# Kernel tuning notes

Measured on AMD Instinct MI355X. Metric: run time of the kernel, lower is better.

Reference implementation:

```python
import jax, jax.numpy as jnp
import numpy as np

EMBED_DIM = 512
NUM_HEADS = 8
HEAD_DIM = EMBED_DIM // NUM_HEADS  # 64


def setup_inputs() -> dict:
    key = jax.random.key(0)
    ks = jax.random.split(key, 9)
    B, N, E, H, D = 4, 1024, EMBED_DIM, NUM_HEADS, HEAD_DIM
    s = 1.0 / np.sqrt(E)  # ~ nn.Linear init scale
    x = jax.random.normal(ks[0], (B, N, E), dtype=jnp.float32)
    # weights stored as (in, out): y = x @ W + b (same math as torch x @ W.T)
    Wq = jax.random.uniform(ks[1], (E, E), jnp.float32, -s, s)
    bq = jax.random.uniform(ks[2], (E,), jnp.float32, -s, s)
    Wk = jax.random.uniform(ks[3], (E, E), jnp.float32, -s, s)
    bk = jax.random.uniform(ks[4], (E,), jnp.float32, -s, s)
    Wv = jax.random.uniform(ks[5], (E, E), jnp.float32, -s, s)
    bv = jax.random.uniform(ks[6], (E,), jnp.float32, -s, s)
    Wg = jax.random.uniform(ks[7], (E, H * D * D), jnp.float32, -s, s)
    bg = jax.random.uniform(ks[8], (H * D * D,), jnp.float32, -s, s)
    return {"x": x, "Wq": Wq, "bq": bq, "Wk": Wk, "bk": bk,
            "Wv": Wv, "bv": bv, "Wg": Wg, "bg": bg}


def reference(x, Wq, bq, Wk, bk, Wv, bv, Wg, bg):
    B, N, E = x.shape
    H, D = NUM_HEADS, HEAD_DIM
    # per-token generated transform g: [B, N, H, D, D] (act = exact GELU)
    g = jax.nn.gelu(x @ Wg + bg, approximate=False).reshape(B, N, H, D, D)
    q = (x @ Wq + bq).reshape(B, N, H, D)
    k = (x @ Wk + bk).reshape(B, N, H, D)
    v = (x @ Wv + bv).reshape(B, N, H, D)
    # q' = q @ g  (per-token, per-head 1xD @ DxD)
    qg = jnp.einsum("bnhd,bnhde->bnhe", q, g)
    # attention scores (note: no 1/sqrt(d) scaling in the original)
    att = jnp.einsum("bnhe,bmhe->bhnm", qg, k)
    att = jax.nn.softmax(att, axis=-1)
    out = jnp.einsum("bhnm,bmhd->bnhd", att, v)
    return out.reshape(B, N, E)
```

## Files before the change

### kernel.cpp

```cpp
#include <hip/hip_runtime.h>
#include <math.h>

#define TOK   4096
#define EDIM  512
#define HEADS 8
#define DHEAD 64
#define GCOLS 32768

typedef unsigned short u16;
typedef _Float16 f16;
typedef __attribute__((ext_vector_type(8))) f16 f16x8;
typedef __attribute__((ext_vector_type(4))) f16 f16x4;
typedef __attribute__((ext_vector_type(4))) float f32x4;
typedef __attribute__((ext_vector_type(4))) unsigned short u16x4;

typedef const __attribute__((address_space(1))) void* gas_ptr;
typedef __attribute__((address_space(3))) void* las_ptr;

__device__ __forceinline__ void gll16(const void* g, void* lds) {
  __builtin_amdgcn_global_load_lds((gas_ptr)g, (las_ptr)lds, 16, 0, 0);
}

#define WAITV(N) asm volatile("s_waitcnt vmcnt(" #N ")" ::: "memory")
__device__ __forceinline__ void barrier_raw() { asm volatile("s_barrier" ::: "memory"); }

__device__ __forceinline__ u16 f2h_bits(float f) {
  union { f16 h; u16 u; } v; v.h = (f16)f;
  return v.u;
}

__device__ __forceinline__ float fast_gelu(float x) {
  float s = x * 0.7071067811865475f;
  float ax = fabsf(s);
  float t = __builtin_amdgcn_rcpf(1.0f + 0.3275911f * ax);
  float poly = t * (0.254829592f + t * (-0.284496736f + t * (1.421413741f +
               t * (-1.453152027f + t * 1.061405429f))));
  float e = __expf(-ax * ax);
  float r = 1.0f - poly * e;
  float erfv = copysignf(r, s);
  return 0.5f * x * (1.0f + erfv);
}

__global__ void cast_f16_k(const float* __restrict__ in, u16* __restrict__ out, int n) {
  int i = (blockIdx.x * blockDim.x + threadIdx.x) * 4;
  if (i + 3 < n) {
    float4 f = *(const float4*)(in + i);
    u16x4 h;
    h.x = f2h_bits(f.x); h.y = f2h_bits(f.y);
    h.z = f2h_bits(f.z); h.w = f2h_bits(f.w);
    *(u16x4*)(out + i) = h;
  }
}

__global__ void transpose_f16_k(const float* __restrict__ in, u16* __restrict__ out,
                                int K, int N) {
  __shared__ float tile[32][33];
  int n0 = blockIdx.x * 32, k0 = blockIdx.y * 32;
  int tx = threadIdx.x, ty = threadIdx.y;
  #pragma unroll
  for (int i = 0; i < 4; i++)
    tile[ty + i * 8][tx] = in[(size_t)(k0 + ty + i * 8) * N + n0 + tx];
  __syncthreads();
  #pragma unroll
  for (int i = 0; i < 4; i++)
    out[(size_t)(n0 + ty + i * 8) * K + k0 + tx] = f2h_bits(tile[tx][ty + i * 8]);
}

__global__ __launch_bounds__(256, 2) void qkv_gemm_k(
    const u16* __restrict__ xf, const u16* __restrict__ Wqt,
    const u16* __restrict__ Wkt, const u16* __restrict__ Wvt,
    const float* __restrict__ bq, const float* __restrict__ bk, const float* __restrict__ bv,
    u16* __restrict__ qho, u16* __restrict__ ko, u16* __restrict__ vTo) {
  __shared__ __align__(16) u16 As[2][16 * 512];
  __shared__ __align__(16) u16 Bs[2][16 * 512];
  const int which = blockIdx.z;
  const u16* Wt = which == 0 ? Wqt : (which == 1 ? Wkt : Wvt);
  const float* bias = which == 0 ? bq : (which == 1 ? bk : bv);
  const int m0 = blockIdx.x * 128;
  const int n0 = blockIdx.y * 128;
  const int tid = threadIdx.x;
  const int w = tid >> 6, lane = tid & 63, l15 = lane & 15, quad = lane >> 4;
  const int mhalf = w >> 1, nhalf = w & 1;

  f32x4 acc[4][4];
  #pragma unroll
  for (int i = 0; i < 4; i++)
    #pragma unroll
    for (int j = 0; j < 4; j++) acc[i][j] = f32x4{0.f, 0.f, 0.f, 0.f};

  auto stage = [&](int d, int kk) {
    #pragma unroll
    for (int i = 0; i < 8; i++) {
      int cb = w * 8 + i;
      if (cb < 16) {
        int ks = cb >> 3, mt = cb & 7;
        gll16(xf + (size_t)(m0 + mt * 16 + l15) * 512 + kk + ks * 32 + quad * 8,
              As[d] + cb * 512);
      } else {
        int bi = cb - 16, ks = bi >> 3, nt = bi & 7;
        gll16(Wt + (size_t)(n0 + nt * 16 + l15) * 512 + kk + ks * 32 + quad * 8,
              Bs[d] + bi * 512);
      }
    }
  };

  stage(0, 0);
  int cur = 0;
  for (int kt = 0; kt < 8; kt++) {
    if (kt < 7) { stage(cur ^ 1, (kt + 1) * 64); WAITV(8); }
    else        { WAITV(0); }
    barrier_raw();
    const u16* Asb = As[cur];
    const u16* Bsb = Bs[cur];
    #pragma unroll
    for (int ks = 0; ks < 2; ks++) {
      f16x8 a[4], b[4];
      #pragma unroll
      for (int mt = 0; mt < 4; mt++)
        a[mt] = *(const f16x8*)(Asb + (ks * 8 + mhalf * 4 + mt) * 512 + lane * 8);
      #pragma unroll
      for (int nt = 0; nt < 4; nt++)
        b[nt] = *(const f16x8*)(Bsb + (ks * 8 + nhalf * 4 + nt) * 512 + lane * 8);
      #pragma unroll
      for (int mt = 0; mt < 4; mt++)
        #pragma unroll
        for (int nt = 0; nt < 4; nt++)
          acc[mt][nt] = __builtin_amdgcn_mfma_f32_16x16x32_f16(a[mt], b[nt], acc[mt][nt], 0, 0, 0);
    }
    barrier_raw();
    cur ^= 1;
  }
  #pragma unroll
  for (int nt = 0; nt < 4; nt++) {
    int col = n0 + (nhalf * 4 + nt) * 16 + l15;
    float bia = bias[col];
    int h = col >> 6, d = col & 63;
    #pragma unroll
    for (int mt = 0; mt < 4; mt++) {
      #pragma unroll
      for (int r = 0; r < 4; r++) {
        int t = m0 + (mhalf * 4 + mt) * 16 + quad * 4 + r;
        int b_ = t >> 10, n = t & 1023;
        float val = acc[mt][nt][r] + bia;
        size_t idx = (((size_t)(b_ * 8 + h) * 1024) + n) * 64 + d;
        if (which == 0)      qho[idx] = f2h_bits(val);
        else if (which == 1) ko[idx] = f2h_bits(val);
        else                 vTo[(((size_t)(b_ * 8 + h) * 64) + d) * 1024 + n] = f2h_bits(val);
      }
    }
  }
}

__global__ __launch_bounds__(512, 2) void qg_fused_k(
    const u16* __restrict__ xf, const u16* __restrict__ Wgt,
    const float* __restrict__ bg, const u16* __restrict__ qh,
    u16* __restrict__ qg16) {
  __shared__ __align__(16) u16 As[2][16 * 512];
  __shared__ __align__(16) u16 Bs[2][32 * 512];
  __shared__ __align__(16) u16 Qs[128 * 64];
  __shared__ __align__(16) float bgs[4096];
  const int head = blockIdx.x & 7;
  const int t0 = (blockIdx.x >> 3) * 128;
  const int tid = threadIdx.x;
  const int w = tid >> 6, lane = tid & 63, l15 = lane & 15, quad = lane >> 4;
  const int mhalf = w >> 2;
  const int ntA = w & 3;
  const int b_ = t0 >> 10, nseq0 = t0 & 1023;
  const u16* qbase = qh + (((size_t)(b_ * 8 + head) * 1024) + nseq0) * 64;
  const float* bgbase = bg + head * 4096;

  #pragma unroll
  for (int i = 0; i < 2; i++) {
    int cb = w * 2 + i;
    gll16(qbase + (size_t)cb * 512 + (size_t)lane * 8, Qs + (size_t)cb * 512);
    gll16(bgbase + (size_t)cb * 256 + (size_t)lane * 4, bgs + (size_t)cb * 256);
  }

  auto stage = [&](int d, int s) {
    int jp = s >> 3, kk = (s & 7) << 6;
    int c0 = head * 4096 + jp * 256;
    #pragma unroll
    for (int i = 0; i < 6; i++) {
      int cb = w * 6 + i;
      if (cb < 16) {
        int ks = cb >> 3, mt = cb & 7;
        gll16(xf + (size_t)(t0 + mt * 16 + l15) * 512 + kk + ks * 32 + quad * 8,
              As[d] + cb * 512);
      } else {
        int bi = cb - 16, ks = bi >> 4, nt = bi & 15;
        gll16(Wgt + (size_t)(c0 + nt * 16 + l15) * 512 + kk + ks * 32 + quad * 8,
              Bs[d] + bi * 512);
      }
    }
  };

  f32x4 qg[4];
  #pragma unroll
  for (int i = 0; i < 4; i++) qg[i] = f32x4{0.f, 0.f, 0.f, 0.f};
  f32x4 zacc[4][4];
  #pragma unroll
  for (int i = 0; i < 4; i++)
    #pragma unroll
    for (int z = 0; z < 4; z++) zacc[i][z] = f32x4{0.f, 0.f, 0.f, 0.f};

  stage(0, 0);
  int cur = 0;
  for (int s = 0; s < 128; s++) {
    if (s < 127) { stage(cur ^ 1, s + 1); WAITV(6); }
    else         { WAITV(0); }
    barrier_raw();
    const u16* Asb = As[cur];
    const u16* Bsb = Bs[cur];
    #pragma unroll
    for (int ks = 0; ks < 2; ks++) {
      f16x8 a[4];
      #pragma unroll
      for (int mt = 0; mt < 4; mt++)
        a[mt] = *(const f16x8*)(Asb + (ks * 8 + mhalf * 4 + mt) * 512 + lane * 8);
      #pragma unroll
      for (int z = 0; z < 4; z++) {
        int nt = (z >> 1) * 8 + (z & 1) * 4 + ntA;
        f16x8 b = *(const f16x8*)(Bsb + (ks * 16 + nt) * 512 + lane * 8);
        #pragma unroll
        for (int mt = 0; mt < 4; mt++)
          zacc[mt][z] = __builtin_amdgcn_mfma_f32_16x16x32_f16(a[mt], b, zacc[mt][z], 0, 0, 0);
      }
    }
    if ((s & 7) == 7) {
      int jp = s >> 3;
      float bgv[4];
      #pragma unroll
      for (int z = 0; z < 4; z++) {
        int nt = (z >> 1) * 8 + (z & 1) * 4 + ntA;
        bgv[z] = bgs[jp * 256 + nt * 16 + l15];
      }
      const int d0 = 4 * jp;
      #pragma unroll
      for (int mt = 0; mt < 4; mt++) {
        #pragma unroll
        for (int r = 0; r < 4; r++) {
          int row = mhalf * 64 + mt * 16 + quad * 4 + r;
          f16x4 qp = *(const f16x4*)(Qs + row * 64 + d0);
          float g0 = fast_gelu(zacc[mt][0][r] + bgv[0]);
          float g1 = fast_gelu(zacc[mt][1][r] + bgv[1]);
          float g2 = fast_gelu(zacc[mt][2][r] + bgv[2]);
          float g3 = fast_gelu(zacc[mt][3][r] + bgv[3]);
          qg[mt][r] += (float)qp.x * g0 + (float)qp.y * g1 +
                       (float)qp.z * g2 + (float)qp.w * g3;
        }
      }
      #pragma unroll
      for (int i = 0; i < 4; i++)
        #pragma unroll
        for (int z = 0; z < 4; z++) zacc[i][z] = f32x4{0.f, 0.f, 0.f, 0.f};
    }
    barrier_raw();
    cur ^= 1;
  }
  const int eb = ntA * 16;
  #pragma unroll
  for (int mt = 0; mt < 4; mt++) {
    #pragma unroll
    for (int r = 0; r < 4; r++) {
      int t = t0 + mhalf * 64 + mt * 16 + quad * 4 + r;
      int bb = t >> 10, n = t & 1023;
      qg16[(((size_t)(bb * 8 + head) * 1024) + n) * 64 + eb + l15] = f2h_bits(qg[mt][r]);
    }
  }
}

__global__ __launch_bounds__(256, 2) void attn_k(
    const u16* __restrict__ qg16, const u16* __restrict__ kb,
    const u16* __restrict__ vTb, float* __restrict__ out) {
  __shared__ __align__(16) u16 Ks[2][8 * 512];
  __shared__ __align__(16) u16 Vs[2][8 * 512];
  __shared__ __align__(16) f16 Ps[4][16 * 72];
  const int idx = blockIdx.x;
  const int bh = idx & 31;
  const int qt = idx >> 5;
  const int b_ = bh >> 3, h = bh & 7;
  const int tid = threadIdx.x;
  const int w = tid >> 6, lane = tid & 63, l15 = lane & 15, quad = lane >> 4;

  const u16* qgB = qg16 + (size_t)bh * 1024 * 64;
  const u16* kB  = kb  + (size_t)bh * 1024 * 64;
  const u16* vB  = vTb + (size_t)bh * 64 * 1024;

  f16x8 aq[2];
  #pragma unroll
  for (int ks = 0; ks < 2; ks++)
    aq[ks] = *(const f16x8*)(qgB + (size_t)(qt * 64 + w * 16 + l15) * 64 + ks * 32 + quad * 8);

  f32x4 o[4];
  #pragma unroll
  for (int i = 0; i < 4; i++) o[i] = f32x4{0.f, 0.f, 0.f, 0.f};
  float m_old[4], l_old[4];
  #pragma unroll
  for (int r = 0; r < 4; r++) { m_old[r] = -1e30f; l_old[r] = 0.f; }

  auto stageKV = [&](int d, int kt) {
    #pragma unroll
    for (int i = 0; i < 2; i++) {
      int cb = w * 2 + i;
      int ks = cb >> 2, nt = cb & 3;
      gll16(kB + (size_t)(kt * 64 + nt * 16 + l15) * 64 + ks * 32 + quad * 8, Ks[d] + cb * 512);
      gll16(vB + (size_t)(nt * 16 + l15) * 1024 + kt * 64 + ks * 32 + quad * 8, Vs[d] + cb * 512);
    }
  };

  stageKV(0, 0);
  int cur = 0;
  for (int kt = 0; kt < 16; kt++) {
    if (kt < 15) { stageKV(cur ^ 1, kt + 1); WAITV(4); }
    else         { WAITV(0); }
    barrier_raw();
    f32x4 s[4];
    #pragma unroll
    for (int nt = 0; nt < 4; nt++) s[nt] = f32x4{0.f, 0.f, 0.f, 0.f};
    #pragma unroll
    for (int ks = 0; ks < 2; ks++)
      #pragma unroll
      for (int nt = 0; nt < 4; nt++) {
        f16x8 kf = *(const f16x8*)(Ks[cur] + (ks * 4 + nt) * 512 + lane * 8);
        s[nt] = __builtin_amdgcn_mfma_f32_16x16x32_f16(aq[ks], kf, s[nt], 0, 0, 0);
      }
    float rmax[4];
    #pragma unroll
    for (int r = 0; r < 4; r++)
      rmax[r] = fmaxf(fmaxf(s[0][r], s[1][r]), fmaxf(s[2][r], s[3][r]));
    #pragma unroll
    for (int off = 1; off < 16; off <<= 1)
      #pragma unroll
      for (int r = 0; r < 4; r++)
        rmax[r] = fmaxf(rmax[r], __shfl_xor(rmax[r], off));
    float alpha[4], rsum[4];
    #pragma unroll
    for (int r = 0; r < 4; r++) {
      float mn = fmaxf(m_old[r], rmax[r]);
      alpha[r] = __expf(m_old[r] - mn);
      m_old[r] = mn;
      rsum[r] = 0.f;
    }
    #pragma unroll
    for (int nt = 0; nt < 4; nt++)
      #pragma unroll
      for (int r = 0; r < 4; r++) {
        float p = __expf(s[nt][r] - m_old[r]);
        rsum[r] += p;
        Ps[w][(quad * 4 + r) * 72 + nt * 16 + l15] = (f16)p;
      }
    #pragma unroll
    for (int off = 1; off < 16; off <<= 1)
      #pragma unroll
      for (int r = 0; r < 4; r++)
        rsum[r] += __shfl_xor(rsum[r], off);
    #pragma unroll
    for (int r = 0; r < 4; r++) l_old[r] = l_old[r] * alpha[r] + rsum[r];
    #pragma unroll
    for (int nt = 0; nt < 4; nt++)
      #pragma unroll
      for (int r = 0; r < 4; r++) o[nt][r] *= alpha[r];
    #pragma unroll
    for (int ks = 0; ks < 2; ks++) {
      f16x8 pa = *(const f16x8*)(&Ps[w][l15 * 72 + ks * 32 + quad * 8]);
      #pragma unroll
      for (int nt = 0; nt < 4; nt++) {
        f16x8 vf = *(const f16x8*)(Vs[cur] + (ks * 4 + nt) * 512 + lane * 8);
        o[nt] = __builtin_amdgcn_mfma_f32_16x16x32_f16(pa, vf, o[nt], 0, 0, 0);
      }
    }
    barrier_raw();
    cur ^= 1;
  }
  #pragma unroll
  for (int r = 0; r < 4; r++) {
    float inv = 1.f / l_old[r];
    int n = qt * 64 + w * 16 + quad * 4 + r;
    #pragma unroll
    for (int nt = 0; nt < 4; nt++)
      out[((size_t)(b_ * 1024 + n)) * 512 + h * 64 + nt * 16 + l15] = o[nt][r] * inv;
  }
}

extern "C" void kernel_launch(void* const* d_in, const int* in_sizes, int n_in,
                              void* d_out, int out_size, void* d_ws, size_t ws_size,
                              hipStream_t stream) {
  const float* x  = (const float*)d_in[0];
  const float* Wq = (const float*)d_in[1];
  const float* bq = (const float*)d_in[2];
  const float* Wk = (const float*)d_in[3];
  const float* bk = (const float*)d_in[4];
  const float* Wv = (const float*)d_in[5];
  const float* bv = (const float*)d_in[6];
  const float* Wg = (const float*)d_in[7];
  const float* bg = (const float*)d_in[8];
  float* out = (float*)d_out;

  const size_t NX = (size_t)TOK * EDIM;
  const size_t NWG = (size_t)GCOLS * EDIM;
  const size_t NW = (size_t)EDIM * EDIM;

  char* p = (char*)d_ws;
  u16* xf  = (u16*)p; p += NX * 2;
  u16* Wgt = (u16*)p; p += NWG * 2;
  u16* Wqt = (u16*)p; p += NW * 2;
  u16* Wkt = (u16*)p; p += NW * 2;
  u16* Wvt = (u16*)p; p += NW * 2;
  u16* qh  = (u16*)p; p += NX * 2;
  u16* kf  = (u16*)p; p += NX * 2;
  u16* vT  = (u16*)p; p += NX * 2;
  u16* qg16 = (u16*)p; p += NX * 2;

  hipLaunchKernelGGL(cast_f16_k, dim3(NX / 1024), dim3(256), 0, stream,
                     x, xf, (int)NX);
  hipLaunchKernelGGL(transpose_f16_k, dim3(EDIM / 32, EDIM / 32), dim3(32, 8), 0, stream,
                     Wq, Wqt, EDIM, EDIM);
  hipLaunchKernelGGL(transpose_f16_k, dim3(EDIM / 32, EDIM / 32), dim3(32, 8), 0, stream,
                     Wk, Wkt, EDIM, EDIM);
  hipLaunchKernelGGL(transpose_f16_k, dim3(EDIM / 32, EDIM / 32), dim3(32, 8), 0, stream,
                     Wv, Wvt, EDIM, EDIM);
  hipLaunchKernelGGL(transpose_f16_k, dim3(GCOLS / 32, EDIM / 32), dim3(32, 8), 0, stream,
                     Wg, Wgt, EDIM, GCOLS);
  hipLaunchKernelGGL(qkv_gemm_k, dim3(TOK / 128, EDIM / 128, 3), dim3(256), 0, stream,
                     xf, Wqt, Wkt, Wvt, bq, bk, bv, qh, kf, vT);
  hipLaunchKernelGGL(qg_fused_k, dim3(256), dim3(512), 0, stream,
                     xf, Wgt, bg, qh, qg16);
  hipLaunchKernelGGL(attn_k, dim3(512), dim3(256), 0, stream,
                     qg16, kf, vT, out);
}
```

Baseline: 429.5 us.

## Triple-buffer Wg tiles with prefetch distance two and drop second barrier

Restructures the main loop of the fused q·g kernel so the Wg tile stream is triple-buffered with a prefetch distance of two steps, while the x tile stays double-buffered. Loads are now issued after the barrier, which removes the trailing per-iteration barrier. To free LDS for the extra buffer, bg is pre-cast to fp16 by an added cast launch and held in shared memory as half precision. This trades a little bias precision and one extra small kernel for deeper latency hiding of global loads. With the loop peeling, the last steps redundantly reload tile 127.

```diff
diff --git a/kernel.cpp b/kernel.cpp
--- a/kernel.cpp
+++ b/kernel.cpp
@@ -153,12 +153,12 @@
 
 __global__ __launch_bounds__(512, 2) void qg_fused_k(
     const u16* __restrict__ xf, const u16* __restrict__ Wgt,
-    const float* __restrict__ bg, const u16* __restrict__ qh,
+    const u16* __restrict__ bgh, const u16* __restrict__ qh,
     u16* __restrict__ qg16) {
   __shared__ __align__(16) u16 As[2][16 * 512];
-  __shared__ __align__(16) u16 Bs[2][32 * 512];
+  __shared__ __align__(16) u16 Bs[3][32 * 512];
   __shared__ __align__(16) u16 Qs[128 * 64];
-  __shared__ __align__(16) float bgs[4096];
+  __shared__ __align__(16) f16 bgs[4096];
   const int head = blockIdx.x & 7;
   const int t0 = (blockIdx.x >> 3) * 128;
   const int tid = threadIdx.x;
@@ -167,32 +167,38 @@
   const int ntA = w & 3;
   const int b_ = t0 >> 10, nseq0 = t0 & 1023;
   const u16* qbase = qh + (((size_t)(b_ * 8 + head) * 1024) + nseq0) * 64;
-  const float* bgbase = bg + head * 4096;
+
+  auto stageA = [&](int d, int s) {
+    int kk = (s & 7) << 6;
+    #pragma unroll
+    for (int i = 0; i < 2; i++) {
+      int cb = w * 2 + i;
+      int ks = cb >> 3, mt = cb & 7;
+      gll16(xf + (size_t)(t0 + mt * 16 + l15) * 512 + kk + ks * 32 + quad * 8,
+            As[d] + cb * 512);
+    }
+  };
+  auto stageB = [&](int d, int s) {
+    int jp = s >> 3, kk = (s & 7) << 6;
+    int c0 = head * 4096 + jp * 256;
+    #pragma unroll
+    for (int i = 0; i < 4; i++) {
+      int bi = w * 4 + i;
+      int ks = bi >> 4, nt = bi & 15;
+      gll16(Wgt + (size_t)(c0 + nt * 16 + l15) * 512 + kk + ks * 32 + quad * 8,
+            Bs[d] + bi * 512);
+    }
+  };
 
   #pragma unroll
   for (int i = 0; i < 2; i++) {
     int cb = w * 2 + i;
     gll16(qbase + (size_t)cb * 512 + (size_t)lane * 8, Qs + (size_t)cb * 512);
-    gll16(bgbase + (size_t)cb * 256 + (size_t)lane * 4, bgs + (size_t)cb * 256);
-  }
-
-  auto stage = [&](int d, int s) {
-    int jp = s >> 3, kk = (s & 7) << 6;
-    int c0 = head * 4096 + jp * 256;
-    #pragma unroll
-    for (int i = 0; i < 6; i++) {
-      int cb = w * 6 + i;
-      if (cb < 16) {
-        int ks = cb >> 3, mt = cb & 7;
-        gll16(xf + (size_t)(t0 + mt * 16 + l15) * 512 + kk + ks * 32 + quad * 8,
-              As[d] + cb * 512);
-      } else {
-        int bi = cb - 16, ks = bi >> 4, nt = bi & 15;
-        gll16(Wgt + (size_t)(c0 + nt * 16 + l15) * 512 + kk + ks * 32 + quad * 8,
-              Bs[d] + bi * 512);
-      }
-    }
-  };
+  }
+  gll16(bgh + (size_t)head * 4096 + w * 512 + lane * 8, bgs + w * 512);
+  stageA(0, 0);
+  stageB(0, 0);
+  stageB(1, 1);
 
   f32x4 qg[4];
   #pragma unroll
@@ -203,14 +209,19 @@
     #pragma unroll
     for (int z = 0; z < 4; z++) zacc[i][z] = f32x4{0.f, 0.f, 0.f, 0.f};
 
-  stage(0, 0);
-  int cur = 0;
+  int acur = 0, bcur = 0;
   for (int s = 0; s < 128; s++) {
-    if (s < 127) { stage(cur ^ 1, s + 1); WAITV(6); }
-    else         { WAITV(0); }
+    WAITV(4);
     barrier_raw();
-    const u16* Asb = As[cur];
-    const u16* Bsb = Bs[cur];
+    {
+      int sa = s + 1 < 128 ? s + 1 : 127;
+      int sb = s + 2 < 128 ? s + 2 : 127;
+      stageA(acur ^ 1, sa);
+      int bw = bcur == 0 ? 2 : bcur - 1;
+      stageB(bw, sb);
+    }
+    const u16* Asb = As[acur];
+    const u16* Bsb = Bs[bcur];
     #pragma unroll
     for (int ks = 0; ks < 2; ks++) {
       f16x8 a[4];
@@ -232,7 +243,7 @@
       #pragma unroll
       for (int z = 0; z < 4; z++) {
         int nt = (z >> 1) * 8 + (z & 1) * 4 + ntA;
-        bgv[z] = bgs[jp * 256 + nt * 16 + l15];
+        bgv[z] = (float)bgs[jp * 256 + nt * 16 + l15];
       }
       const int d0 = 4 * jp;
       #pragma unroll
@@ -254,9 +265,10 @@
         #pragma unroll
         for (int z = 0; z < 4; z++) zacc[i][z] = f32x4{0.f, 0.f, 0.f, 0.f};
     }
-    barrier_raw();
-    cur ^= 1;
-  }
+    acur ^= 1;
+    bcur = bcur == 2 ? 0 : bcur + 1;
+  }
+  WAITV(0);
   const int eb = ntA * 16;
   #pragma unroll
   for (int mt = 0; mt < 4; mt++) {
@@ -410,9 +422,12 @@
   u16* kf  = (u16*)p; p += NX * 2;
   u16* vT  = (u16*)p; p += NX * 2;
   u16* qg16 = (u16*)p; p += NX * 2;
+  u16* bgh = (u16*)p; p += GCOLS * 2;
 
   hipLaunchKernelGGL(cast_f16_k, dim3(NX / 1024), dim3(256), 0, stream,
                      x, xf, (int)NX);
+  hipLaunchKernelGGL(cast_f16_k, dim3(GCOLS / 1024), dim3(256), 0, stream,
+                     bg, bgh, GCOLS);
   hipLaunchKernelGGL(transpose_f16_k, dim3(EDIM / 32, EDIM / 32), dim3(32, 8), 0, stream,
                      Wq, Wqt, EDIM, EDIM);
   hipLaunchKernelGGL(transpose_f16_k, dim3(EDIM / 32, EDIM / 32), dim3(32, 8), 0, stream,
@@ -424,7 +439,7 @@
   hipLaunchKernelGGL(qkv_gemm_k, dim3(TOK / 128, EDIM / 128, 3), dim3(256), 0, stream,
                      xf, Wqt, Wkt, Wvt, bq, bk, bv, qh, kf, vT);
   hipLaunchKernelGGL(qg_fused_k, dim3(256), dim3(512), 0, stream,
-                     xf, Wgt, bg, qh, qg16);
+                     xf, Wgt, bgh, qh, qg16);
   hipLaunchKernelGGL(attn_k, dim3(512), dim3(256), 0, stream,
                      qg16, kf, vT, out);
 }
```

Result: slower. 501.3 us (+16.7%).

## Split qg fused GEMM over d-quarters with fp32 partials reduced in attention

Applied to the files above, without the earlier changes.

The qg fused kernel now splits each head's D dimension into four quarters across separate blocks (1024 blocks of 256 threads instead of 256 of 512). Each block writes fp32 partial q@g results, and the attention kernel sums the four partials when loading Q. The bias is pre-cast to f16 by an extra cast launch, and the two N-halves are reduced within the block through LDS. This is meant to raise parallelism and occupancy for the dominant GEMM, at the cost of four times as much fp32 partial-result traffic and scalar strided loads in attention.

```diff
diff --git a/kernel.cpp b/kernel.cpp
--- a/kernel.cpp
+++ b/kernel.cpp
@@ -151,126 +151,141 @@
   }
 }
 
-__global__ __launch_bounds__(512, 2) void qg_fused_k(
+__global__ __launch_bounds__(256, 2) void qg_fused_k(
     const u16* __restrict__ xf, const u16* __restrict__ Wgt,
-    const float* __restrict__ bg, const u16* __restrict__ qh,
-    u16* __restrict__ qg16) {
+    const u16* __restrict__ bgh, const u16* __restrict__ qh,
+    float* __restrict__ qgp) {
   __shared__ __align__(16) u16 As[2][16 * 512];
-  __shared__ __align__(16) u16 Bs[2][32 * 512];
-  __shared__ __align__(16) u16 Qs[128 * 64];
-  __shared__ __align__(16) float bgs[4096];
-  const int head = blockIdx.x & 7;
-  const int t0 = (blockIdx.x >> 3) * 128;
+  __shared__ __align__(16) u16 Bs[2][16 * 512];
+  __shared__ __align__(16) f16 Qs[128 * 16];
+  __shared__ __align__(16) f16 bgs[16 * 64];
+  const int bid = blockIdx.x;
+  const int dq = bid & 3, head = (bid >> 2) & 7;
+  const int t0 = (bid >> 5) * 128;
   const int tid = threadIdx.x;
   const int w = tid >> 6, lane = tid & 63, l15 = lane & 15, quad = lane >> 4;
-  const int mhalf = w >> 2;
-  const int ntA = w & 3;
+  const int mhalf = w >> 1, nhalf = w & 1;
   const int b_ = t0 >> 10, nseq0 = t0 & 1023;
-  const u16* qbase = qh + (((size_t)(b_ * 8 + head) * 1024) + nseq0) * 64;
-  const float* bgbase = bg + head * 4096;
+  const int bh = b_ * 8 + head;
+  const u16* qbase = qh + (((size_t)bh * 1024) + nseq0) * 64;
 
   #pragma unroll
   for (int i = 0; i < 2; i++) {
-    int cb = w * 2 + i;
-    gll16(qbase + (size_t)cb * 512 + (size_t)lane * 8, Qs + (size_t)cb * 512);
-    gll16(bgbase + (size_t)cb * 256 + (size_t)lane * 4, bgs + (size_t)cb * 256);
+    int job = w * 2 + i; if (job >= 6) job -= 6;
+    if (job < 4) {
+      gll16(qbase + (size_t)(job * 32 + (lane >> 1)) * 64 + dq * 16 + (lane & 1) * 8,
+            (f16*)Qs + job * 512);
+    } else {
+      int j = job - 4;
+      gll16(bgh + (size_t)head * 4096 + (dq * 16 + j * 8 + (lane >> 3)) * 64 + (lane & 7) * 8,
+            (f16*)bgs + j * 512);
+    }
   }
 
   auto stage = [&](int d, int s) {
     int jp = s >> 3, kk = (s & 7) << 6;
-    int c0 = head * 4096 + jp * 256;
-    #pragma unroll
-    for (int i = 0; i < 6; i++) {
-      int cb = w * 6 + i;
-      if (cb < 16) {
-        int ks = cb >> 3, mt = cb & 7;
-        gll16(xf + (size_t)(t0 + mt * 16 + l15) * 512 + kk + ks * 32 + quad * 8,
-              As[d] + cb * 512);
-      } else {
-        int bi = cb - 16, ks = bi >> 4, nt = bi & 15;
-        gll16(Wgt + (size_t)(c0 + nt * 16 + l15) * 512 + kk + ks * 32 + quad * 8,
-              Bs[d] + bi * 512);
-      }
+    const u16* bsrc = Wgt + (size_t)(head * 4096 + (dq * 16 + jp * 2) * 64) * 512;
+    #pragma unroll
+    for (int i = 0; i < 4; i++) {
+      int cb = w * 4 + i, ks = cb >> 3, mt = cb & 7;
+      gll16(xf + (size_t)(t0 + mt * 16 + l15) * 512 + kk + ks * 32 + quad * 8,
+            As[d] + cb * 512);
+    }
+    #pragma unroll
+    for (int i = 0; i < 4; i++) {
+      int bi = w * 4 + i, ks = bi >> 3, nt = bi & 7;
+      gll16(bsrc + (size_t)(nt * 16 + l15) * 512 + kk + ks * 32 + quad * 8,
+            Bs[d] + bi * 512);
     }
   };
 
-  f32x4 qg[4];
-  #pragma unroll
-  for (int i = 0; i < 4; i++) qg[i] = f32x4{0.f, 0.f, 0.f, 0.f};
-  f32x4 zacc[4][4];
+  f32x4 acc[4][4], qgacc[4][4];
   #pragma unroll
   for (int i = 0; i < 4; i++)
     #pragma unroll
-    for (int z = 0; z < 4; z++) zacc[i][z] = f32x4{0.f, 0.f, 0.f, 0.f};
+    for (int j = 0; j < 4; j++) {
+      acc[i][j] = f32x4{0.f, 0.f, 0.f, 0.f};
+      qgacc[i][j] = f32x4{0.f, 0.f, 0.f, 0.f};
+    }
 
   stage(0, 0);
-  int cur = 0;
-  for (int s = 0; s < 128; s++) {
-    if (s < 127) { stage(cur ^ 1, s + 1); WAITV(6); }
-    else         { WAITV(0); }
-    barrier_raw();
-    const u16* Asb = As[cur];
-    const u16* Bsb = Bs[cur];
+  for (int s = 0; s < 64; s++) {
+    if (s < 63) { stage((s + 1) & 1, s + 1); WAITV(8); }
+    else        { WAITV(0); }
+    barrier_raw();
+    const u16* Asb = As[s & 1];
+    const u16* Bsb = Bs[s & 1];
     #pragma unroll
     for (int ks = 0; ks < 2; ks++) {
-      f16x8 a[4];
+      f16x8 a[4], b[4];
       #pragma unroll
       for (int mt = 0; mt < 4; mt++)
         a[mt] = *(const f16x8*)(Asb + (ks * 8 + mhalf * 4 + mt) * 512 + lane * 8);
       #pragma unroll
-      for (int z = 0; z < 4; z++) {
-        int nt = (z >> 1) * 8 + (z & 1) * 4 + ntA;
-        f16x8 b = *(const f16x8*)(Bsb + (ks * 16 + nt) * 512 + lane * 8);
-        #pragma unroll
-        for (int mt = 0; mt < 4; mt++)
-          zacc[mt][z] = __builtin_amdgcn_mfma_f32_16x16x32_f16(a[mt], b, zacc[mt][z], 0, 0, 0);
-      }
+      for (int nt = 0; nt < 4; nt++)
+        b[nt] = *(const f16x8*)(Bsb + (ks * 8 + nhalf * 4 + nt) * 512 + lane * 8);
+      #pragma unroll
+      for (int mt = 0; mt < 4; mt++)
+        #pragma unroll
+        for (int nt = 0; nt < 4; nt++)
+          acc[mt][nt] = __builtin_amdgcn_mfma_f32_16x16x32_f16(a[mt], b[nt], acc[mt][nt], 0, 0, 0);
     }
     if ((s & 7) == 7) {
       int jp = s >> 3;
+      int dloc = jp * 2 + nhalf;
       float bgv[4];
       #pragma unroll
-      for (int z = 0; z < 4; z++) {
-        int nt = (z >> 1) * 8 + (z & 1) * 4 + ntA;
-        bgv[z] = bgs[jp * 256 + nt * 16 + l15];
-      }
-      const int d0 = 4 * jp;
+      for (int nt = 0; nt < 4; nt++)
+        bgv[nt] = (float)bgs[dloc * 64 + nt * 16 + l15];
       #pragma unroll
       for (int mt = 0; mt < 4; mt++) {
         #pragma unroll
         for (int r = 0; r < 4; r++) {
           int row = mhalf * 64 + mt * 16 + quad * 4 + r;
-          f16x4 qp = *(const f16x4*)(Qs + row * 64 + d0);
-          float g0 = fast_gelu(zacc[mt][0][r] + bgv[0]);
-          float g1 = fast_gelu(zacc[mt][1][r] + bgv[1]);
-          float g2 = fast_gelu(zacc[mt][2][r] + bgv[2]);
-          float g3 = fast_gelu(zacc[mt][3][r] + bgv[3]);
-          qg[mt][r] += (float)qp.x * g0 + (float)qp.y * g1 +
-                       (float)qp.z * g2 + (float)qp.w * g3;
+          float qv = (float)Qs[row * 16 + dloc];
+          #pragma unroll
+          for (int nt = 0; nt < 4; nt++)
+            qgacc[mt][nt][r] += qv * fast_gelu(acc[mt][nt][r] + bgv[nt]);
         }
       }
       #pragma unroll
       for (int i = 0; i < 4; i++)
         #pragma unroll
-        for (int z = 0; z < 4; z++) zacc[i][z] = f32x4{0.f, 0.f, 0.f, 0.f};
-    }
-    barrier_raw();
-    cur ^= 1;
-  }
-  const int eb = ntA * 16;
-  #pragma unroll
-  for (int mt = 0; mt < 4; mt++) {
-    #pragma unroll
-    for (int r = 0; r < 4; r++) {
-      int t = t0 + mhalf * 64 + mt * 16 + quad * 4 + r;
-      int bb = t >> 10, n = t & 1023;
-      qg16[(((size_t)(bb * 8 + head) * 1024) + n) * 64 + eb + l15] = f2h_bits(qg[mt][r]);
-    }
+        for (int j = 0; j < 4; j++) acc[i][j] = f32x4{0.f, 0.f, 0.f, 0.f};
+    }
+    barrier_raw();
+  }
+  float* red = (float*)As;
+  if (nhalf == 1) {
+    #pragma unroll
+    for (int mt = 0; mt < 4; mt++)
+      #pragma unroll
+      for (int r = 0; r < 4; r++) {
+        int tok = mhalf * 64 + mt * 16 + quad * 4 + r;
+        #pragma unroll
+        for (int nt = 0; nt < 4; nt++)
+          red[tok * 64 + nt * 16 + l15] = qgacc[mt][nt][r];
+      }
+  }
+  barrier_raw();
+  if (nhalf == 0) {
+    float* outp = qgp + ((size_t)dq * 32 + bh) * 1024 * 64;
+    #pragma unroll
+    for (int mt = 0; mt < 4; mt++)
+      #pragma unroll
+      for (int r = 0; r < 4; r++) {
+        int tok = mhalf * 64 + mt * 16 + quad * 4 + r;
+        int n = nseq0 + tok;
+        #pragma unroll
+        for (int nt = 0; nt < 4; nt++)
+          outp[(size_t)n * 64 + nt * 16 + l15] =
+              qgacc[mt][nt][r] + red[tok * 64 + nt * 16 + l15];
+      }
   }
 }
 
 __global__ __launch_bounds__(256, 2) void attn_k(
-    const u16* __restrict__ qg16, const u16* __restrict__ kb,
+    const float* __restrict__ qgp, const u16* __restrict__ kb,
     const u16* __restrict__ vTb, float* __restrict__ out) {
   __shared__ __align__(16) u16 Ks[2][8 * 512];
   __shared__ __align__(16) u16 Vs[2][8 * 512];
@@ -282,14 +297,22 @@
   const int tid = threadIdx.x;
   const int w = tid >> 6, lane = tid & 63, l15 = lane & 15, quad = lane >> 4;
 
-  const u16* qgB = qg16 + (size_t)bh * 1024 * 64;
+  const float* qgB = qgp + (size_t)bh * 1024 * 64;
+  const size_t PS = (size_t)32 * 1024 * 64;
   const u16* kB  = kb  + (size_t)bh * 1024 * 64;
   const u16* vB  = vTb + (size_t)bh * 64 * 1024;
 
   f16x8 aq[2];
   #pragma unroll
-  for (int ks = 0; ks < 2; ks++)
-    aq[ks] = *(const f16x8*)(qgB + (size_t)(qt * 64 + w * 16 + l15) * 64 + ks * 32 + quad * 8);
+  for (int ks = 0; ks < 2; ks++) {
+    size_t off = (size_t)(qt * 64 + w * 16 + l15) * 64 + ks * 32 + quad * 8;
+    f16x8 v;
+    #pragma unroll
+    for (int e = 0; e < 8; e++)
+      v[e] = (f16)(qgB[off + e] + qgB[PS + off + e] +
+                   qgB[2 * PS + off + e] + qgB[3 * PS + off + e]);
+    aq[ks] = v;
+  }
 
   f32x4 o[4];
   #pragma unroll
@@ -409,10 +432,13 @@
   u16* qh  = (u16*)p; p += NX * 2;
   u16* kf  = (u16*)p; p += NX * 2;
   u16* vT  = (u16*)p; p += NX * 2;
-  u16* qg16 = (u16*)p; p += NX * 2;
+  float* qgp = (float*)p; p += NX * 4 * 4;
+  u16* bgh = (u16*)p; p += GCOLS * 2;
 
   hipLaunchKernelGGL(cast_f16_k, dim3(NX / 1024), dim3(256), 0, stream,
                      x, xf, (int)NX);
+  hipLaunchKernelGGL(cast_f16_k, dim3(GCOLS / 1024), dim3(256), 0, stream,
+                     bg, bgh, GCOLS);
   hipLaunchKernelGGL(transpose_f16_k, dim3(EDIM / 32, EDIM / 32), dim3(32, 8), 0, stream,
                      Wq, Wqt, EDIM, EDIM);
   hipLaunchKernelGGL(transpose_f16_k, dim3(EDIM / 32, EDIM / 32), dim3(32, 8), 0, stream,
@@ -423,8 +449,8 @@
                      Wg, Wgt, EDIM, GCOLS);
   hipLaunchKernelGGL(qkv_gemm_k, dim3(TOK / 128, EDIM / 128, 3), dim3(256), 0, stream,
                      xf, Wqt, Wkt, Wvt, bq, bk, bv, qh, kf, vT);
-  hipLaunchKernelGGL(qg_fused_k, dim3(256), dim3(512), 0, stream,
-                     xf, Wgt, bg, qh, qg16);
+  hipLaunchKernelGGL(qg_fused_k, dim3(1024), dim3(256), 0, stream,
+                     xf, Wgt, bgh, qh, qgp);
   hipLaunchKernelGGL(attn_k, dim3(512), dim3(256), 0, stream,
-                     qg16, kf, vT, out);
-}
+                     qgp, kf, vT, out);
+}
```

New measurement: 464.6 us. 1.08x slower.

## Split qg fused kernel across d-halves with fp32 partials and single-buffered LDS

Applied to the files above, without the earlier changes.

Splits the per-head q@g reduction over the D dimension into two halves, doubling the qg grid to 512 blocks, each writing fp32 partial sums that attention adds together when loading q. LDS is single-buffered and bias is pre-cast to fp16 so that more blocks fit per CU (launch bounds raised to 4). The aim is to fill the GPU better than 256 blocks do. The cost is losing the double-buffered load/compute overlap, extra fp32 partial traffic, and unvectorised scalar loads in attention.

```diff
diff --git a/kernel.cpp b/kernel.cpp
--- a/kernel.cpp
+++ b/kernel.cpp
@@ -151,45 +151,48 @@
   }
 }
 
-__global__ __launch_bounds__(512, 2) void qg_fused_k(
+__global__ __launch_bounds__(512, 4) void qg_fused_k(
     const u16* __restrict__ xf, const u16* __restrict__ Wgt,
-    const float* __restrict__ bg, const u16* __restrict__ qh,
-    u16* __restrict__ qg16) {
-  __shared__ __align__(16) u16 As[2][16 * 512];
-  __shared__ __align__(16) u16 Bs[2][32 * 512];
-  __shared__ __align__(16) u16 Qs[128 * 64];
-  __shared__ __align__(16) float bgs[4096];
-  const int head = blockIdx.x & 7;
-  const int t0 = (blockIdx.x >> 3) * 128;
+    const u16* __restrict__ bgh, const u16* __restrict__ qh,
+    float* __restrict__ qgp) {
+  __shared__ __align__(16) u16 As[16 * 512];
+  __shared__ __align__(16) u16 Bs[32 * 512];
+  __shared__ __align__(16) f16 Qs[128 * 32];
+  __shared__ __align__(16) f16 bgs[32 * 64];
+  const int bid = blockIdx.x;
+  const int head = bid & 7;
+  const int dh = (bid >> 3) & 1;
+  const int t0 = (bid >> 4) * 128;
   const int tid = threadIdx.x;
   const int w = tid >> 6, lane = tid & 63, l15 = lane & 15, quad = lane >> 4;
   const int mhalf = w >> 2;
   const int ntA = w & 3;
   const int b_ = t0 >> 10, nseq0 = t0 & 1023;
-  const u16* qbase = qh + (((size_t)(b_ * 8 + head) * 1024) + nseq0) * 64;
-  const float* bgbase = bg + head * 4096;
-
-  #pragma unroll
-  for (int i = 0; i < 2; i++) {
-    int cb = w * 2 + i;
-    gll16(qbase + (size_t)cb * 512 + (size_t)lane * 8, Qs + (size_t)cb * 512);
-    gll16(bgbase + (size_t)cb * 256 + (size_t)lane * 4, bgs + (size_t)cb * 256);
-  }
-
-  auto stage = [&](int d, int s) {
+  const int bh = b_ * 8 + head;
+  const u16* qbase = qh + (((size_t)bh * 1024) + nseq0) * 64;
+
+  {
+    gll16(qbase + (size_t)(w * 16 + (lane >> 2)) * 64 + dh * 32 + (lane & 3) * 8,
+          (f16*)Qs + w * 512);
+    int c = w & 3;
+    gll16(bgh + (size_t)head * 4096 + (size_t)(dh * 32 + c * 8 + (lane >> 3)) * 64 + (lane & 7) * 8,
+          (f16*)bgs + c * 512);
+  }
+
+  auto stage = [&](int s) {
     int jp = s >> 3, kk = (s & 7) << 6;
-    int c0 = head * 4096 + jp * 256;
+    int c0 = head * 4096 + (dh * 32 + jp * 4) * 64;
     #pragma unroll
     for (int i = 0; i < 6; i++) {
       int cb = w * 6 + i;
       if (cb < 16) {
         int ks = cb >> 3, mt = cb & 7;
         gll16(xf + (size_t)(t0 + mt * 16 + l15) * 512 + kk + ks * 32 + quad * 8,
-              As[d] + cb * 512);
+              As + cb * 512);
       } else {
         int bi = cb - 16, ks = bi >> 4, nt = bi & 15;
         gll16(Wgt + (size_t)(c0 + nt * 16 + l15) * 512 + kk + ks * 32 + quad * 8,
-              Bs[d] + bi * 512);
+              Bs + bi * 512);
       }
     }
   };
@@ -203,24 +206,19 @@
     #pragma unroll
     for (int z = 0; z < 4; z++) zacc[i][z] = f32x4{0.f, 0.f, 0.f, 0.f};
 
-  stage(0, 0);
-  int cur = 0;
-  for (int s = 0; s < 128; s++) {
-    if (s < 127) { stage(cur ^ 1, s + 1); WAITV(6); }
-    else         { WAITV(0); }
-    barrier_raw();
-    const u16* Asb = As[cur];
-    const u16* Bsb = Bs[cur];
+  for (int s = 0; s < 64; s++) {
+    stage(s);
+    __syncthreads();
     #pragma unroll
     for (int ks = 0; ks < 2; ks++) {
       f16x8 a[4];
       #pragma unroll
       for (int mt = 0; mt < 4; mt++)
-        a[mt] = *(const f16x8*)(Asb + (ks * 8 + mhalf * 4 + mt) * 512 + lane * 8);
+        a[mt] = *(const f16x8*)(As + (ks * 8 + mhalf * 4 + mt) * 512 + lane * 8);
       #pragma unroll
       for (int z = 0; z < 4; z++) {
         int nt = (z >> 1) * 8 + (z & 1) * 4 + ntA;
-        f16x8 b = *(const f16x8*)(Bsb + (ks * 16 + nt) * 512 + lane * 8);
+        f16x8 b = *(const f16x8*)(Bs + (ks * 16 + nt) * 512 + lane * 8);
         #pragma unroll
         for (int mt = 0; mt < 4; mt++)
           zacc[mt][z] = __builtin_amdgcn_mfma_f32_16x16x32_f16(a[mt], b, zacc[mt][z], 0, 0, 0);
@@ -230,17 +228,15 @@
       int jp = s >> 3;
       float bgv[4];
       #pragma unroll
-      for (int z = 0; z < 4; z++) {
-        int nt = (z >> 1) * 8 + (z & 1) * 4 + ntA;
-        bgv[z] = bgs[jp * 256 + nt * 16 + l15];
-      }
-      const int d0 = 4 * jp;
+      for (int z = 0; z < 4; z++)
+        bgv[z] = (float)bgs[(jp * 4 + z) * 64 + ntA * 16 + l15];
+      const int d0 = jp * 4;
       #pragma unroll
       for (int mt = 0; mt < 4; mt++) {
         #pragma unroll
         for (int r = 0; r < 4; r++) {
           int row = mhalf * 64 + mt * 16 + quad * 4 + r;
-          f16x4 qp = *(const f16x4*)(Qs + row * 64 + d0);
+          f16x4 qp = *(const f16x4*)(Qs + row * 32 + d0);
           float g0 = fast_gelu(zacc[mt][0][r] + bgv[0]);
           float g1 = fast_gelu(zacc[mt][1][r] + bgv[1]);
           float g2 = fast_gelu(zacc[mt][2][r] + bgv[2]);
@@ -254,23 +250,23 @@
         #pragma unroll
         for (int z = 0; z < 4; z++) zacc[i][z] = f32x4{0.f, 0.f, 0.f, 0.f};
     }
-    barrier_raw();
-    cur ^= 1;
-  }
+    __syncthreads();
+  }
+  float* outp = qgp + (size_t)dh * TOK * 512 + ((size_t)bh * 1024) * 64;
   const int eb = ntA * 16;
   #pragma unroll
   for (int mt = 0; mt < 4; mt++) {
     #pragma unroll
     for (int r = 0; r < 4; r++) {
-      int t = t0 + mhalf * 64 + mt * 16 + quad * 4 + r;
-      int bb = t >> 10, n = t & 1023;
-      qg16[(((size_t)(bb * 8 + head) * 1024) + n) * 64 + eb + l15] = f2h_bits(qg[mt][r]);
+      int tok = mhalf * 64 + mt * 16 + quad * 4 + r;
+      int n = nseq0 + tok;
+      outp[(size_t)n * 64 + eb + l15] = qg[mt][r];
     }
   }
 }
 
 __global__ __launch_bounds__(256, 2) void attn_k(
-    const u16* __restrict__ qg16, const u16* __restrict__ kb,
+    const float* __restrict__ qgp, const u16* __restrict__ kb,
     const u16* __restrict__ vTb, float* __restrict__ out) {
   __shared__ __align__(16) u16 Ks[2][8 * 512];
   __shared__ __align__(16) u16 Vs[2][8 * 512];
@@ -282,14 +278,21 @@
   const int tid = threadIdx.x;
   const int w = tid >> 6, lane = tid & 63, l15 = lane & 15, quad = lane >> 4;
 
-  const u16* qgB = qg16 + (size_t)bh * 1024 * 64;
+  const float* qg0 = qgp + ((size_t)bh * 1024) * 64;
+  const float* qg1 = qg0 + (size_t)TOK * 512;
   const u16* kB  = kb  + (size_t)bh * 1024 * 64;
   const u16* vB  = vTb + (size_t)bh * 64 * 1024;
 
   f16x8 aq[2];
   #pragma unroll
-  for (int ks = 0; ks < 2; ks++)
-    aq[ks] = *(const f16x8*)(qgB + (size_t)(qt * 64 + w * 16 + l15) * 64 + ks * 32 + quad * 8);
+  for (int ks = 0; ks < 2; ks++) {
+    size_t off = (size_t)(qt * 64 + w * 16 + l15) * 64 + ks * 32 + quad * 8;
+    f16x8 v;
+    #pragma unroll
+    for (int e = 0; e < 8; e++)
+      v[e] = (f16)(qg0[off + e] + qg1[off + e]);
+    aq[ks] = v;
+  }
 
   f32x4 o[4];
   #pragma unroll
@@ -409,10 +412,13 @@
   u16* qh  = (u16*)p; p += NX * 2;
   u16* kf  = (u16*)p; p += NX * 2;
   u16* vT  = (u16*)p; p += NX * 2;
-  u16* qg16 = (u16*)p; p += NX * 2;
+  float* qgp = (float*)p; p += NX * 4 * 2;
+  u16* bgh = (u16*)p; p += GCOLS * 2;
 
   hipLaunchKernelGGL(cast_f16_k, dim3(NX / 1024), dim3(256), 0, stream,
                      x, xf, (int)NX);
+  hipLaunchKernelGGL(cast_f16_k, dim3(GCOLS / 1024), dim3(256), 0, stream,
+                     bg, bgh, GCOLS);
   hipLaunchKernelGGL(transpose_f16_k, dim3(EDIM / 32, EDIM / 32), dim3(32, 8), 0, stream,
                      Wq, Wqt, EDIM, EDIM);
   hipLaunchKernelGGL(transpose_f16_k, dim3(EDIM / 32, EDIM / 32), dim3(32, 8), 0, stream,
@@ -423,8 +429,8 @@
                      Wg, Wgt, EDIM, GCOLS);
   hipLaunchKernelGGL(qkv_gemm_k, dim3(TOK / 128, EDIM / 128, 3), dim3(256), 0, stream,
                      xf, Wqt, Wkt, Wvt, bq, bk, bv, qh, kf, vT);
-  hipLaunchKernelGGL(qg_fused_k, dim3(256), dim3(512), 0, stream,
-                     xf, Wgt, bg, qh, qg16);
+  hipLaunchKernelGGL(qg_fused_k, dim3(512), dim3(512), 0, stream,
+                     xf, Wgt, bgh, qh, qgp);
   hipLaunchKernelGGL(attn_k, dim3(512), dim3(256), 0, stream,
-                     qg16, kf, vT, out);
-}
+                     qgp, kf, vT, out);
+}
```

Measured after the change: 507.1 us. +18.1%, slower.
